# Performance work log

Measured on AMD Instinct MI355X. Metric: run time of the kernel, lower is better.

The kernel has to match this reference:

```python
import jax, jax.numpy as jnp
import numpy as np

# Constants from the module
PROT_RADII = jnp.array([1.7, 1.55, 1.52, 1.8], dtype=jnp.float32)  # prot_radii_map buffer
ALPHA = 1.0          # current_alpha (== ff_params.softness_start)
STEP_PROGRESS = 0.0  # forward kwarg default -> ghost term active, t_gate = sigmoid(-2)
CUTOFF = 12.0
DIELECTRIC = 4.0


def setup_inputs() -> dict:
    key = jax.random.key(0)
    ks = jax.random.split(key, 8)
    B, NL, NP = 8, 128, 8192
    # positions scaled so pairwise distances span a realistic 0-40 A range
    pos_L = jax.random.normal(ks[0], (B, NL, 3), dtype=jnp.float32) * 5.0
    pos_P = jax.random.normal(ks[1], (B, NP, 3), dtype=jnp.float32) * 15.0
    q_L = jax.random.normal(ks[2], (B, NL), dtype=jnp.float32) * 0.3
    q_P = jax.random.normal(ks[3], (B, NP), dtype=jnp.float32) * 0.3
    x_L = jax.random.uniform(ks[4], (B, NL, 9), dtype=jnp.float32)   # ligand type probs (first 9 used)
    x_P = jax.random.uniform(ks[5], (B, NP, 4), dtype=jnp.float32)   # protein class probs (first 4 used)
    vdw_radii = 1.0 + jax.random.uniform(ks[6], (9,), dtype=jnp.float32)   # ~1.0-2.0 A
    epsilon = 0.2 * jax.random.uniform(ks[7], (9,), dtype=jnp.float32)     # well depths
    return dict(pos_L=pos_L, pos_P=pos_P, q_L=q_L, q_P=q_P,
                x_L=x_L, x_P=x_P, vdw_radii=vdw_radii, epsilon=epsilon)


def reference(pos_L, pos_P, q_L, q_P, x_L, x_P, vdw_radii, epsilon):
    # pairwise distances: [B, NL, NP]
    diff = pos_L[:, :, None, :] - pos_P[:, None, :, :]
    dist_sq = jnp.sum(diff * diff, axis=-1)
    dist = jnp.sqrt(dist_sq + 1e-8)

    # mixed vdw radii
    radii_L = x_L @ vdw_radii            # [B, NL]
    radii_P = x_P @ PROT_RADII           # [B, NP]
    sigma_ij = radii_L[:, :, None] + radii_P[:, None, :]

    # softened distance
    soft_dist = jnp.sqrt(dist_sq + ALPHA * sigma_ij * sigma_ij + 1e-8)

    # Coulomb
    e_elec = 332.06 * q_L[:, :, None] * q_P[:, None, :] / (DIELECTRIC * soft_dist)

    # LJ 12-6 with soft clamps
    eps_L = jax.nn.relu(x_L @ epsilon)                    # [B, NL]
    eps_ij = jnp.sqrt(eps_L[:, :, None] * 0.15 + 1e-8)    # [B, NL, 1] broadcast
    ratio = jnp.minimum(sigma_ij / (soft_dist + 1e-8), 5.0)
    ratio6 = ratio ** 6
    ratio12 = ratio6 * ratio6
    e_vdw_raw = 4.0 * eps_ij * (ratio12 - ratio6)
    e_vdw_grad = jax.nn.softplus(e_vdw_raw + 10.0) - 10.0            # soft lower clamp at -10
    e_vdw_grad = -jax.nn.softplus(-(e_vdw_grad - 500.0)) + 500.0     # soft upper clamp at 500

    # smooth cutoff mask
    dist_mask = jax.nn.sigmoid((CUTOFF - dist) * 2.0)
    e_soft = jnp.sum((e_elec + e_vdw_grad) * dist_mask, axis=(1, 2))

    # hydrophobic surface area (carbon-carbon attraction)
    mask_cc = x_L[..., 0][:, :, None] * x_P[..., 0][:, None, :]
    hsa_term = 1.0 / (1.0 + (dist / 4.0) ** 4)
    e_hsa = jnp.sum(-0.5 * mask_cc * hsa_term * dist_mask, axis=(1, 2))

    # Pauli repulsion with time gate
    t_gate = jax.nn.sigmoid(jnp.float32((STEP_PROGRESS - 0.2) * 10.0))
    overlap = jax.nn.relu(sigma_ij * 0.6 - dist)
    e_pauli = t_gate * 100.0 * jnp.sum(overlap * overlap, axis=(1, 2))

    # ghost repulsion (step_progress < 0.15 -> active; static Python branch)
    ghost = jax.nn.relu(0.5 - dist)
    e_ghost = 500.0 * jnp.sum(ghost * ghost, axis=(1, 2))

    e_raw = e_soft + 5.0 * e_hsa + e_pauli + e_ghost

    # logging branch with hard clamps
    log_vdw = jnp.clip(e_vdw_raw, -10.0, 500.0)
    log_soft = jnp.sum((e_elec + log_vdw) * dist_mask, axis=(1, 2)) + 5.0 * e_hsa
    e_soft_final = jnp.clip(log_soft, -500.0, 5000.0)
    e_hard_final = jnp.minimum(e_pauli + e_ghost, 10000.0)
    log_energy = jnp.minimum(e_soft_final + e_hard_final, 1000000.0)

    return e_raw, e_hard_final, log_energy
```

## Files before the change

kernel.cpp:

```cpp
#include <hip/hip_runtime.h>


#define NB 8
#define NL 128
#define NP 8192
#define JT 256
#define JPT 2
#define JB (NP / (JT * JPT))
#define KSEG 8
#define IPER (NL / KSEG)

__global__ __launch_bounds__(JT, 4) void pair_kernel(
    const float* __restrict__ pos_L, const float* __restrict__ pos_P,
    const float* __restrict__ q_L,  const float* __restrict__ q_P,
    const float* __restrict__ x_L,  const float* __restrict__ x_P,
    const float* __restrict__ vdw_radii, const float* __restrict__ epsilon,
    float* __restrict__ part)
{
    __shared__ float4 sA[IPER];
    __shared__ float4 sB[IPER];
    __shared__ float4 red[4];

    const int tid  = threadIdx.x;
    const int b    = blockIdx.x / (JB * KSEG);
    const int rem  = blockIdx.x % (JB * KSEG);
    const int jb   = rem / KSEG;
    const int kseg = rem % KSEG;

    if (tid < IPER) {
        const int i = kseg * IPER + tid;
        const float* xl = x_L + ((size_t)b * NL + i) * 9;
        float rl = 0.f, el = 0.f;
        #pragma unroll
        for (int k = 0; k < 9; ++k) { rl += xl[k] * vdw_radii[k]; el += xl[k] * epsilon[k]; }
        el = fmaxf(el, 0.f);
        const float* pl = pos_L + ((size_t)b * NL + i) * 3;
        sA[tid] = make_float4(pl[0], pl[1], pl[2], 83.015f * q_L[(size_t)b * NL + i]);
        sB[tid] = make_float4(rl, 4.0f * __builtin_amdgcn_sqrtf(el * 0.15f + 1e-8f), xl[0], 0.f);
    }
    __syncthreads();

    const int j0 = jb * (JT * JPT) + tid;
    const int j1 = j0 + JT;
    const float* pp0 = pos_P + ((size_t)b * NP + j0) * 3;
    const float* pp1 = pos_P + ((size_t)b * NP + j1) * 3;
    const float px0 = pp0[0], py0 = pp0[1], pz0 = pp0[2];
    const float px1 = pp1[0], py1 = pp1[1], pz1 = pp1[2];
    const float qp0 = q_P[(size_t)b * NP + j0];
    const float qp1 = q_P[(size_t)b * NP + j1];
    const float4 xpA = *(const float4*)(x_P + ((size_t)b * NP + j0) * 4);
    const float4 xpB = *(const float4*)(x_P + ((size_t)b * NP + j1) * 4);
    const float radP0 = xpA.x * 1.7f + xpA.y * 1.55f + xpA.z * 1.52f + xpA.w * 1.8f;
    const float radP1 = xpB.x * 1.7f + xpB.y * 1.55f + xpB.z * 1.52f + xpB.w * 1.8f;
    const float xp00 = xpA.x, xp01 = xpB.x;

    float a_ev = 0.f;
    float a_el0 = 0.f, a_el1 = 0.f;
    float a_h0 = 0.f, a_h1 = 0.f;
    float a_pau = 0.f, a_gho = 0.f;

    #pragma unroll
    for (int i = 0; i < IPER; ++i) {
        const float4 A = sA[i];
        const float4 Bv = sB[i];

        #pragma unroll
        for (int jj = 0; jj < JPT; ++jj) {
            const float px = jj ? px1 : px0, py = jj ? py1 : py0, pz = jj ? pz1 : pz0;
            const float radP = jj ? radP1 : radP0;

            const float dx = px - A.x, dy = py - A.y, dz = pz - A.z;
            const float d2p = dx * dx + dy * dy + dz * dz + 1e-8f;
            const float dist = __builtin_amdgcn_sqrtf(d2p);
            const float sig = Bv.x + radP;
            const float inv_soft = __builtin_amdgcn_rsqf(__builtin_fmaf(sig, sig, d2p));
            const float ratio = sig * inv_soft;
            const float r2 = ratio * ratio;
            const float r4 = r2 * r2;
            const float r6 = r4 * r2;
            const float evraw = Bv.y * (r6 * (r6 - 1.f));
            const float m = __builtin_amdgcn_rcpf(1.f + __expf(2.f * dist - 24.f));
            a_ev = __builtin_fmaf(evraw, m, a_ev);
            const float elec = A.w * inv_soft;
            if (jj) a_el1 = __builtin_fmaf(elec, m, a_el1);
            else    a_el0 = __builtin_fmaf(elec, m, a_el0);
            const float d4 = d2p * d2p;
            const float hm = __builtin_amdgcn_rcpf(__builtin_fmaf(d4, 1.f / 256.f, 1.f)) * m;
            if (jj) a_h1 = __builtin_fmaf(Bv.z, hm, a_h1);
            else    a_h0 = __builtin_fmaf(Bv.z, hm, a_h0);
            const float ov = fmaxf(__builtin_fmaf(sig, 0.6f, -dist), 0.f);
            a_pau = __builtin_fmaf(ov, ov, a_pau);
            const float gh = fmaxf(0.5f - dist, 0.f);
            a_gho = __builtin_fmaf(gh, gh, a_gho);
        }
    }

    float v0 = a_ev + a_el0 * qp0 + a_el1 * qp1;
    float v1 = a_h0 * xp00 + a_h1 * xp01;
    float v2 = a_pau;
    float v3 = a_gho;

    #pragma unroll
    for (int off = 32; off; off >>= 1) {
        v0 += __shfl_down(v0, off, 64);
        v1 += __shfl_down(v1, off, 64);
        v2 += __shfl_down(v2, off, 64);
        v3 += __shfl_down(v3, off, 64);
    }
    const int wave = tid >> 6;
    if ((tid & 63) == 0) red[wave] = make_float4(v0, v1, v2, v3);
    __syncthreads();
    if (tid == 0) {
        float4 s;
        s.x = red[0].x + red[1].x + red[2].x + red[3].x;
        s.y = red[0].y + red[1].y + red[2].y + red[3].y;
        s.z = red[0].z + red[1].z + red[2].z + red[3].z;
        s.w = red[0].w + red[1].w + red[2].w + red[3].w;
        ((float4*)part)[blockIdx.x] = s;
    }
}

__global__ __launch_bounds__(128) void finalize_kernel(
    const float* __restrict__ part, float* __restrict__ out)
{
    const int b = blockIdx.x;
    const int t = threadIdx.x;
    float4 v = ((const float4*)part)[b * (JB * KSEG) + t];
    #pragma unroll
    for (int off = 32; off; off >>= 1) {
        v.x += __shfl_down(v.x, off, 64);
        v.y += __shfl_down(v.y, off, 64);
        v.z += __shfl_down(v.z, off, 64);
        v.w += __shfl_down(v.w, off, 64);
    }
    __shared__ float4 sh[2];
    if ((t & 63) == 0) sh[t >> 6] = v;
    __syncthreads();
    if (t == 0) {
        const float ev  = sh[0].x + sh[1].x;
        const float hsa = sh[0].y + sh[1].y;
        const float pau = sh[0].z + sh[1].z;
        const float gho = sh[0].w + sh[1].w;
        const float e_hsa5  = -2.5f * hsa;
        const float e_pauli = 11.920292202211755f * pau;
        const float e_ghost = 500.f * gho;
        const float e_raw   = ev + e_hsa5 + e_pauli + e_ghost;
        const float log_soft = ev + e_hsa5;
        const float e_soft_final = fminf(fmaxf(log_soft, -500.f), 5000.f);
        const float e_hard = fminf(e_pauli + e_ghost, 10000.f);
        const float log_energy = fminf(e_soft_final + e_hard, 1000000.f);
        out[b]          = e_raw;
        out[NB + b]     = e_hard;
        out[2 * NB + b] = log_energy;
    }
}

extern "C" void kernel_launch(void* const* d_in, const int* in_sizes, int n_in,
                              void* d_out, int out_size, void* d_ws, size_t ws_size,
                              hipStream_t stream) {
    const float* pos_L = (const float*)d_in[0];
    const float* pos_P = (const float*)d_in[1];
    const float* q_L   = (const float*)d_in[2];
    const float* q_P   = (const float*)d_in[3];
    const float* x_L   = (const float*)d_in[4];
    const float* x_P   = (const float*)d_in[5];
    const float* vdw   = (const float*)d_in[6];
    const float* eps   = (const float*)d_in[7];
    float* part = (float*)d_ws;

    const int grid = NB * JB * KSEG;
    pair_kernel<<<grid, JT, 0, stream>>>(pos_L, pos_P, q_L, q_P, x_L, x_P, vdw, eps, part);
    finalize_kernel<<<NB, 128, 0, stream>>>(part, (float*)d_out);
}
```

Baseline: 81.54 us.

## Fuse sigmoid and HSA reciprocals into one rcp, use exp2, widen j-tiling

Merges the two per-pair reciprocals (distance mask sigmoid and hydrophobic term) into a single rcp of their product, then recovers each factor with a multiply. It also replaces __expf with a direct exp2 using prescaled constants. JPT rises from 2 to 4 and KSEG from 8 to 16, so each thread handles more protein atoms over fewer ligand atoms while the grid size stays the same. This cuts transcendental instructions per pair and raises instruction-level parallelism, but adds registers and makes the product of the two denominators more prone to overflow at large distances.

```diff
diff --git a/kernel.cpp b/kernel.cpp
--- a/kernel.cpp
+++ b/kernel.cpp
@@ -5,10 +5,16 @@
 #define NL 128
 #define NP 8192
 #define JT 256
-#define JPT 2
+#define JPT 4
 #define JB (NP / (JT * JPT))
-#define KSEG 8
+#define KSEG 16
 #define IPER (NL / KSEG)
+
+#if __has_builtin(__builtin_amdgcn_exp2f)
+#define EXP2F(x) __builtin_amdgcn_exp2f(x)
+#else
+#define EXP2F(x) __expf(0.6931471805599453f * (x))
+#endif
 
 __global__ __launch_bounds__(JT, 4) void pair_kernel(
     const float* __restrict__ pos_L, const float* __restrict__ pos_P,
@@ -40,54 +46,48 @@
     }
     __syncthreads();
 
-    const int j0 = jb * (JT * JPT) + tid;
-    const int j1 = j0 + JT;
-    const float* pp0 = pos_P + ((size_t)b * NP + j0) * 3;
-    const float* pp1 = pos_P + ((size_t)b * NP + j1) * 3;
-    const float px0 = pp0[0], py0 = pp0[1], pz0 = pp0[2];
-    const float px1 = pp1[0], py1 = pp1[1], pz1 = pp1[2];
-    const float qp0 = q_P[(size_t)b * NP + j0];
-    const float qp1 = q_P[(size_t)b * NP + j1];
-    const float4 xpA = *(const float4*)(x_P + ((size_t)b * NP + j0) * 4);
-    const float4 xpB = *(const float4*)(x_P + ((size_t)b * NP + j1) * 4);
-    const float radP0 = xpA.x * 1.7f + xpA.y * 1.55f + xpA.z * 1.52f + xpA.w * 1.8f;
-    const float radP1 = xpB.x * 1.7f + xpB.y * 1.55f + xpB.z * 1.52f + xpB.w * 1.8f;
-    const float xp00 = xpA.x, xp01 = xpB.x;
+    const int jbase = jb * (JT * JPT) + tid;
+    float px[JPT], py[JPT], pz[JPT], radP[JPT], qp[JPT], xp0[JPT];
+    #pragma unroll
+    for (int jj = 0; jj < JPT; ++jj) {
+        const int j = jbase + jj * JT;
+        const float* pp = pos_P + ((size_t)b * NP + j) * 3;
+        px[jj] = pp[0]; py[jj] = pp[1]; pz[jj] = pp[2];
+        qp[jj] = q_P[(size_t)b * NP + j];
+        const float4 xp = *(const float4*)(x_P + ((size_t)b * NP + j) * 4);
+        radP[jj] = xp.x * 1.7f + xp.y * 1.55f + xp.z * 1.52f + xp.w * 1.8f;
+        xp0[jj]  = xp.x;
+    }
 
-    float a_ev = 0.f;
-    float a_el0 = 0.f, a_el1 = 0.f;
-    float a_h0 = 0.f, a_h1 = 0.f;
-    float a_pau = 0.f, a_gho = 0.f;
+    float a_ev = 0.f, a_pau = 0.f, a_gho = 0.f;
+    float a_el[JPT] = {0.f, 0.f, 0.f, 0.f};
+    float a_h[JPT]  = {0.f, 0.f, 0.f, 0.f};
 
     #pragma unroll
     for (int i = 0; i < IPER; ++i) {
-        const float4 A = sA[i];
+        const float4 A  = sA[i];
         const float4 Bv = sB[i];
-
         #pragma unroll
         for (int jj = 0; jj < JPT; ++jj) {
-            const float px = jj ? px1 : px0, py = jj ? py1 : py0, pz = jj ? pz1 : pz0;
-            const float radP = jj ? radP1 : radP0;
-
-            const float dx = px - A.x, dy = py - A.y, dz = pz - A.z;
-            const float d2p = dx * dx + dy * dy + dz * dz + 1e-8f;
+            const float dx = px[jj] - A.x, dy = py[jj] - A.y, dz = pz[jj] - A.z;
+            const float d2p = __builtin_fmaf(dx, dx,
+                              __builtin_fmaf(dy, dy,
+                              __builtin_fmaf(dz, dz, 1e-8f)));
             const float dist = __builtin_amdgcn_sqrtf(d2p);
-            const float sig = Bv.x + radP;
+            const float sig  = Bv.x + radP[jj];
             const float inv_soft = __builtin_amdgcn_rsqf(__builtin_fmaf(sig, sig, d2p));
             const float ratio = sig * inv_soft;
             const float r2 = ratio * ratio;
-            const float r4 = r2 * r2;
-            const float r6 = r4 * r2;
-            const float evraw = Bv.y * (r6 * (r6 - 1.f));
-            const float m = __builtin_amdgcn_rcpf(1.f + __expf(2.f * dist - 24.f));
-            a_ev = __builtin_fmaf(evraw, m, a_ev);
-            const float elec = A.w * inv_soft;
-            if (jj) a_el1 = __builtin_fmaf(elec, m, a_el1);
-            else    a_el0 = __builtin_fmaf(elec, m, a_el0);
-            const float d4 = d2p * d2p;
-            const float hm = __builtin_amdgcn_rcpf(__builtin_fmaf(d4, 1.f / 256.f, 1.f)) * m;
-            if (jj) a_h1 = __builtin_fmaf(Bv.z, hm, a_h1);
-            else    a_h0 = __builtin_fmaf(Bv.z, hm, a_h0);
+            const float r6 = r2 * r2 * r2;
+            const float evraw = Bv.y * __builtin_fmaf(r6, r6, -r6);
+            const float e = EXP2F(__builtin_fmaf(dist, 2.8853900817779268f, -34.624680981335123f));
+            const float d4c = __builtin_fmaf(d2p * d2p, 0.00390625f, 1.f);
+            const float P = (1.f + e) * d4c;
+            const float rcpP = __builtin_amdgcn_rcpf(P);
+            const float m = rcpP * d4c;
+            a_ev     = __builtin_fmaf(evraw, m, a_ev);
+            a_el[jj] = __builtin_fmaf(A.w * inv_soft, m, a_el[jj]);
+            a_h[jj]  = __builtin_fmaf(Bv.z, rcpP, a_h[jj]);
             const float ov = fmaxf(__builtin_fmaf(sig, 0.6f, -dist), 0.f);
             a_pau = __builtin_fmaf(ov, ov, a_pau);
             const float gh = fmaxf(0.5f - dist, 0.f);
@@ -95,10 +95,14 @@
         }
     }
 
-    float v0 = a_ev + a_el0 * qp0 + a_el1 * qp1;
-    float v1 = a_h0 * xp00 + a_h1 * xp01;
-    float v2 = a_pau;
-    float v3 = a_gho;
+    float v0 = a_ev;
+    float v1 = 0.f;
+    #pragma unroll
+    for (int jj = 0; jj < JPT; ++jj) {
+        v0 = __builtin_fmaf(a_el[jj], qp[jj], v0);
+        v1 = __builtin_fmaf(a_h[jj], xp0[jj], v1);
+    }
+    float v2 = a_pau, v3 = a_gho;
 
     #pragma unroll
     for (int off = 32; off; off >>= 1) {
```

New measurement: 80.97 us. About the same (-0.7%).
